# Optimization experiments

Measured on AMD Instinct MI355X. Metric: run time of the kernel, lower is better.

Reference implementation:

```python
import jax, jax.numpy as jnp
import numpy as np

KH, KW = 3, 3   # kernel_size
DH, DW = 2, 2   # stride


def _extract_windows(x):
    """Equivalent of x.unfold(2,KH,DH).unfold(3,KW,DW).view(B,C,H',W',KH*KW).
    Loop is over the KH*KW=9 fixed kernel offsets, not data dims."""
    B, C, H, W = x.shape
    Ho = (H - KH) // DH + 1
    Wo = (W - KW) // DW + 1
    cols = [x[:, :, i:i + DH * Ho:DH, j:j + DW * Wo:DW]
            for i in range(KH) for j in range(KW)]  # row-major (kh,kw) matches torch unfold flatten
    return jnp.stack(cols, axis=-1)  # (B, C, Ho, Wo, KH*KW)


def setup_inputs() -> dict:
    key = jax.random.key(0)
    k1, k2 = jax.random.split(key)
    x = jax.random.normal(k1, (8, 32, 64, 64), dtype=jnp.float32)
    # weight: (1, out_channels, in_channels, H', W', kh*kw) with H'=W'=31
    weight = jax.random.normal(k2, (1, 32, 32, 31, 31, 9), dtype=jnp.float32)
    return {"x": x, "weight": weight}


def reference(x, weight):
    # windows: (B, in, H', W', K); weight[0]: (out, in, H', W', K)
    # out[b,o,p,q] = sum_{i,k} windows[b,i,p,q,k] * weight[0,o,i,p,q,k]
    windows = _extract_windows(x)
    return jnp.einsum('bipqk,oipqk->bopq', windows, weight[0])
```

## Files before the change

kernel.cpp:

```cpp
#include <hip/hip_runtime.h>


#define NPART 246016
#define WS_NEED ((size_t)8 * NPART * 4)

#define GLD4(gp, lp)                                                 \
    __builtin_amdgcn_global_load_lds(                                \
        (const __attribute__((address_space(1))) void*)(gp),         \
        (__attribute__((address_space(3))) void*)(lp), 4, 0, 0)
#define GLD16(gp, lp)                                                \
    __builtin_amdgcn_global_load_lds(                                \
        (const __attribute__((address_space(1))) void*)(gp),         \
        (__attribute__((address_space(3))) void*)(lp), 16, 0, 0)

template <bool USE_WS>
__global__ __launch_bounds__(512, 2) void lc2d_kernel(const float* __restrict__ x,
                                                      const float* __restrict__ wgt,
                                                      float* __restrict__ outOrPart) {
    __shared__ float xs[6144];
    __shared__ float wsb[2][5120];

    const int t  = threadIdx.x;
    const int ol = t & 15;
    const int bh = (t >> 4) & 1;
    const int dq = t >> 5;
    const int bid = blockIdx.x;
    const int p  = bid >> 4;
    const int qg = (bid >> 3) & 1;
    const int ig = bid & 7;
    const int i0 = ig * 4;
    const int q0 = qg << 4;
    const int q  = q0 + dq;
    const int waveBase = t & ~63;

#pragma unroll
    for (int j = 0; j < 3; ++j) {
        const int g  = j * 512 + t;
        const int r  = g >> 4;
        const int cw = (g & 15) << 2;
        const int b  = r / 12;
        const int r2 = r - b * 12;
        const int ii = r2 / 3;
        const int kh = r2 - ii * 3;
        const float* gp = x + (size_t)b * 131072 + (size_t)(i0 + ii) * 4096
                            + (size_t)(2 * p + kh) * 64 + cw;
        GLD16(gp, &xs[4 * (j * 512 + waveBase)]);
    }

    const int lim = (qg == 0) ? 143 : 134;
    const int pqb = p * 279 + q0 * 9;
#define STAGE_W(i, buf)                                                          \
    {                                                                            \
        _Pragma("unroll")                                                        \
        for (int j = 0; j < 10; ++j) {                                           \
            int f = t + j * 512; f = (f < 4639) ? f : 4639;                      \
            const int os  = f / 145;                                             \
            const int off = f - os * 145;                                        \
            const int go  = (off < lim) ? off : lim;                             \
            GLD4(wgt + (size_t)os * 276768 + pqb + go + (size_t)(i) * 8649,      \
                 &wsb[buf][j * 512 + waveBase]);                                 \
        }                                                                        \
    }

    STAGE_W(i0, 0);

    float acc[2][4];
#pragma unroll
    for (int lo = 0; lo < 2; ++lo)
#pragma unroll
        for (int bi = 0; bi < 4; ++bi) acc[lo][bi] = 0.f;

    __syncthreads();

    const int wv0 = ol * 145 + dq * 9;
    const int wv1 = (ol + 16) * 145 + dq * 9;

#pragma unroll 1
    for (int ii = 0; ii < 4; ++ii) {
        const float* wb = wsb[ii & 1];

        if (ii < 3) STAGE_W(i0 + ii + 1, (ii + 1) & 1);

        float wv[2][9];
#pragma unroll
        for (int k = 0; k < 9; ++k) {
            wv[0][k] = wb[wv0 + k];
            wv[1][k] = wb[wv1 + k];
        }

        const int xb = bh * 3072 + ii * 192 + 2 * q0 + 2 * dq;
#pragma unroll
        for (int kh = 0; kh < 3; ++kh) {
#pragma unroll
            for (int bi = 0; bi < 4; ++bi) {
                const int base = xb + bi * 768 + kh * 64;
                const float2 a = *reinterpret_cast<const float2*>(&xs[base]);
                const float c1 = xs[base + 2];
#pragma unroll
                for (int lo = 0; lo < 2; ++lo)
                    acc[lo][bi] += wv[lo][kh * 3 + 0] * a.x
                                 + wv[lo][kh * 3 + 1] * a.y
                                 + wv[lo][kh * 3 + 2] * c1;
            }
        }
        __syncthreads();
    }

    if (q <= 30) {
        const int pq = p * 31 + q;
        if (USE_WS) {
#pragma unroll
            for (int lo = 0; lo < 2; ++lo)
#pragma unroll
                for (int bi = 0; bi < 4; ++bi)
                    outOrPart[((size_t)(ig * 8 + bh * 4 + bi) * 961 + pq) * 32 + ol + lo * 16]
                        = acc[lo][bi];
        } else {
#pragma unroll
            for (int lo = 0; lo < 2; ++lo)
#pragma unroll
                for (int bi = 0; bi < 4; ++bi)
                    atomicAdd(&outOrPart[(((size_t)(bh * 4 + bi) * 32 + ol + lo * 16) * 31 + p) * 31 + q],
                              acc[lo][bi]);
        }
    }
}

__global__ __launch_bounds__(256) void lc2d_reduce(const float* __restrict__ part,
                                                   float* __restrict__ out) {
    const int u = blockIdx.x * 256 + threadIdx.x;
    float s = 0.f;
#pragma unroll
    for (int ig = 0; ig < 8; ++ig) s += part[(size_t)ig * NPART + u];
    const int o = u & 31;
    const int r = u >> 5;
    const int b = r / 961;
    const int pq = r - b * 961;
    out[(size_t)(b * 32 + o) * 961 + pq] = s;
}

extern "C" void kernel_launch(void* const* d_in, const int* in_sizes, int n_in,
                              void* d_out, int out_size, void* d_ws, size_t ws_size,
                              hipStream_t stream) {
    const float* x = (const float*)d_in[0];
    const float* w = (const float*)d_in[1];
    float* out = (float*)d_out;

    if (ws_size >= WS_NEED) {
        float* part = (float*)d_ws;
        lc2d_kernel<true><<<dim3(31 * 2 * 8), dim3(512), 0, stream>>>(x, w, part);
        lc2d_reduce<<<dim3(NPART / 256), dim3(256), 0, stream>>>(part, out);
    } else {
        hipMemsetAsync(out, 0, (size_t)out_size * sizeof(float), stream);
        lc2d_kernel<false><<<dim3(31 * 2 * 8), dim3(512), 0, stream>>>(x, w, out);
    }
}
```

Baseline: 85.03 us.

## Split output channels across blocks and prefetch all weights up front

The grid doubles, and each block now computes 16 output channels instead of 32, so there are more blocks to fill the GPU. Each block loads all four input-channel weight slices into LDS at once instead of double-buffering them. This removes the per-iteration barriers and the staged reloads. In exchange, every block reloads the same x tile and does less compute per block, so x traffic and staging overhead per FLOP go up.

Result: slower. 88.28 us (+3.8%).

```diff
diff --git a/kernel.cpp b/kernel.cpp
--- a/kernel.cpp
+++ b/kernel.cpp
@@ -18,19 +18,21 @@
                                                       const float* __restrict__ wgt,
                                                       float* __restrict__ outOrPart) {
     __shared__ float xs[6144];
-    __shared__ float wsb[2][5120];
+    __shared__ float wlds[4 * 2560];
 
     const int t  = threadIdx.x;
     const int ol = t & 15;
     const int bh = (t >> 4) & 1;
     const int dq = t >> 5;
     const int bid = blockIdx.x;
-    const int p  = bid >> 4;
-    const int qg = (bid >> 3) & 1;
-    const int ig = bid & 7;
+    const int p  = bid >> 5;
+    const int qg = (bid >> 4) & 1;
+    const int ig = (bid >> 1) & 7;
+    const int oh = bid & 1;
     const int i0 = ig * 4;
     const int q0 = qg << 4;
     const int q  = q0 + dq;
+    const int o  = oh * 16 + ol;
     const int waveBase = t & ~63;
 
 #pragma unroll
@@ -49,44 +51,34 @@
 
     const int lim = (qg == 0) ? 143 : 134;
     const int pqb = p * 279 + q0 * 9;
-#define STAGE_W(i, buf)                                                          \
-    {                                                                            \
-        _Pragma("unroll")                                                        \
-        for (int j = 0; j < 10; ++j) {                                           \
-            int f = t + j * 512; f = (f < 4639) ? f : 4639;                      \
-            const int os  = f / 145;                                             \
-            const int off = f - os * 145;                                        \
-            const int go  = (off < lim) ? off : lim;                             \
-            GLD4(wgt + (size_t)os * 276768 + pqb + go + (size_t)(i) * 8649,      \
-                 &wsb[buf][j * 512 + waveBase]);                                 \
-        }                                                                        \
+    const int obase = oh * 16;
+#pragma unroll
+    for (int ii = 0; ii < 4; ++ii) {
+        const size_t iw = (size_t)(i0 + ii) * 8649;
+#pragma unroll
+        for (int j = 0; j < 5; ++j) {
+            int f = t + j * 512; f = (f < 2319) ? f : 2319;
+            const int os  = f / 145;
+            const int off = f - os * 145;
+            const int go  = (off < lim) ? off : lim;
+            GLD4(wgt + (size_t)(obase + os) * 276768 + pqb + go + iw,
+                 &wlds[ii * 2560 + j * 512 + waveBase]);
+        }
     }
 
-    STAGE_W(i0, 0);
-
-    float acc[2][4];
+    float acc[4];
 #pragma unroll
-    for (int lo = 0; lo < 2; ++lo)
-#pragma unroll
-        for (int bi = 0; bi < 4; ++bi) acc[lo][bi] = 0.f;
+    for (int bi = 0; bi < 4; ++bi) acc[bi] = 0.f;
 
     __syncthreads();
 
-    const int wv0 = ol * 145 + dq * 9;
-    const int wv1 = (ol + 16) * 145 + dq * 9;
+    const int wvb = ol * 145 + dq * 9;
 
 #pragma unroll 1
     for (int ii = 0; ii < 4; ++ii) {
-        const float* wb = wsb[ii & 1];
-
-        if (ii < 3) STAGE_W(i0 + ii + 1, (ii + 1) & 1);
-
-        float wv[2][9];
+        float wv[9];
 #pragma unroll
-        for (int k = 0; k < 9; ++k) {
-            wv[0][k] = wb[wv0 + k];
-            wv[1][k] = wb[wv1 + k];
-        }
+        for (int k = 0; k < 9; ++k) wv[k] = wlds[ii * 2560 + wvb + k];
 
         const int xb = bh * 3072 + ii * 192 + 2 * q0 + 2 * dq;
 #pragma unroll
@@ -96,32 +88,23 @@
                 const int base = xb + bi * 768 + kh * 64;
                 const float2 a = *reinterpret_cast<const float2*>(&xs[base]);
                 const float c1 = xs[base + 2];
-#pragma unroll
-                for (int lo = 0; lo < 2; ++lo)
-                    acc[lo][bi] += wv[lo][kh * 3 + 0] * a.x
-                                 + wv[lo][kh * 3 + 1] * a.y
-                                 + wv[lo][kh * 3 + 2] * c1;
+                acc[bi] += wv[kh * 3 + 0] * a.x + wv[kh * 3 + 1] * a.y
+                         + wv[kh * 3 + 2] * c1;
             }
         }
-        __syncthreads();
     }
 
     if (q <= 30) {
         const int pq = p * 31 + q;
         if (USE_WS) {
 #pragma unroll
-            for (int lo = 0; lo < 2; ++lo)
-#pragma unroll
-                for (int bi = 0; bi < 4; ++bi)
-                    outOrPart[((size_t)(ig * 8 + bh * 4 + bi) * 961 + pq) * 32 + ol + lo * 16]
-                        = acc[lo][bi];
+            for (int bi = 0; bi < 4; ++bi)
+                outOrPart[((size_t)(ig * 8 + bh * 4 + bi) * 961 + pq) * 32 + o] = acc[bi];
         } else {
 #pragma unroll
-            for (int lo = 0; lo < 2; ++lo)
-#pragma unroll
-                for (int bi = 0; bi < 4; ++bi)
-                    atomicAdd(&outOrPart[(((size_t)(bh * 4 + bi) * 32 + ol + lo * 16) * 31 + p) * 31 + q],
-                              acc[lo][bi]);
+            for (int bi = 0; bi < 4; ++bi)
+                atomicAdd(&outOrPart[(((size_t)(bh * 4 + bi) * 32 + o) * 31 + p) * 31 + q],
+                          acc[bi]);
         }
     }
 }
@@ -148,10 +131,10 @@
 
     if (ws_size >= WS_NEED) {
         float* part = (float*)d_ws;
-        lc2d_kernel<true><<<dim3(31 * 2 * 8), dim3(512), 0, stream>>>(x, w, part);
+        lc2d_kernel<true><<<dim3(31 * 2 * 8 * 2), dim3(512), 0, stream>>>(x, w, part);
         lc2d_reduce<<<dim3(NPART / 256), dim3(256), 0, stream>>>(part, out);
     } else {
         hipMemsetAsync(out, 0, (size_t)out_size * sizeof(float), stream);
-        lc2d_kernel<false><<<dim3(31 * 2 * 8), dim3(512), 0, stream>>>(x, w, out);
+        lc2d_kernel<false><<<dim3(31 * 2 * 8 * 2), dim3(512), 0, stream>>>(x, w, out);
     }
 }
```
